# Kernel tuning notes

Measured on AMD Instinct MI355X. Metric: run time of the kernel, lower is better.

The kernel has to match this reference:

```python
import jax, jax.numpy as jnp
import numpy as np

S, B, D, H, F = 2048, 4, 1024, 16, 4096
DH = D // H  # per-head dim (nhid)
EPS = 1e-5


def layer_norm(x, g, b):
    m = jnp.mean(x, axis=-1, keepdims=True)
    v = jnp.mean((x - m) ** 2, axis=-1, keepdims=True)
    return (x - m) * jax.lax.rsqrt(v + EPS) * g + b


def setup_inputs() -> dict:
    key = jax.random.key(0)
    ks = jax.random.split(key, 16)
    s = 1.0 / np.sqrt(D)
    sf = 1.0 / np.sqrt(F)
    return {
        "x": jax.random.normal(ks[0], (S, B, D), dtype=jnp.float32),
        "ln1_g": jnp.ones((D,), jnp.float32),
        "ln1_b": jnp.zeros((D,), jnp.float32),
        "ln2_g": jnp.ones((D,), jnp.float32),
        "ln2_b": jnp.zeros((D,), jnp.float32),
        "Wq": jax.random.normal(ks[1], (D, D), jnp.float32) * s,
        "bq": jnp.zeros((D,), jnp.float32),
        "Wk": jax.random.normal(ks[2], (D, D), jnp.float32) * s,
        "bk": jnp.zeros((D,), jnp.float32),
        "Wv": jax.random.normal(ks[3], (D, D), jnp.float32) * s,
        "bv": jnp.zeros((D,), jnp.float32),
        "Wo": jax.random.normal(ks[4], (D, D), jnp.float32) * s,
        "bo": jnp.zeros((D,), jnp.float32),
        "W1": jax.random.normal(ks[5], (D, F), jnp.float32) * s,
        "b1": jnp.zeros((F,), jnp.float32),
        "W2": jax.random.normal(ks[6], (F, D), jnp.float32) * sf,
        "b2": jnp.zeros((D,), jnp.float32),
    }


def reference(x, ln1_g, ln1_b, ln2_g, ln2_b, Wq, bq, Wk, bk, Wv, bv, Wo, bo, W1, b1, W2, b2):
    # --- sublayer 0: LN -> full (non-causal) multi-head self-attention -> residual ---
    h = layer_norm(x, ln1_g, ln1_b)                      # [S,B,D]
    q = (h @ Wq + bq).reshape(S, B, H, DH)
    k = (h @ Wk + bk).reshape(S, B, H, DH)
    v = (h @ Wv + bv).reshape(S, B, H, DH)
    scale = 1.0 / jnp.sqrt(jnp.asarray(DH, x.dtype))
    scores = jnp.einsum("sbhd,tbhd->bhst", q, k) * scale  # [B,H,S,S]
    attn = jax.nn.softmax(scores, axis=-1)
    ctx = jnp.einsum("bhst,tbhd->sbhd", attn, v).reshape(S, B, D)
    x = x + (ctx @ Wo + bo)
    # --- sublayer 1: LN -> position-wise FFN -> residual ---
    h2 = layer_norm(x, ln2_g, ln2_b)
    ff = jax.nn.relu(h2 @ W1 + b1) @ W2 + b2
    return x + ff
```

## Files before the change

### kernel.cpp

```cpp
#include <hip/hip_runtime.h>
#include <hip/hip_bf16.h>
#include <stdint.h>

constexpr int S = 2048;
constexpr int B = 4;
constexpr int D = 1024;
constexpr int H = 16;
constexpr int F = 4096;
constexpr int DH = 64;
constexpr int N = S * B;
constexpr int QKVS = 3 * D;

typedef __attribute__((ext_vector_type(8))) short  bf16x8;
typedef __attribute__((ext_vector_type(4))) float  floatx4;

__device__ __forceinline__ unsigned short f2bf(float f) {
    __hip_bfloat16 h = __float2bfloat16(f);
    return __builtin_bit_cast(unsigned short, h);
}
__device__ __forceinline__ uint32_t pack_bf2_fast(float a, float b) {
    uint32_t ua = __builtin_bit_cast(uint32_t, a) + 0x8000u;
    uint32_t ub = __builtin_bit_cast(uint32_t, b) + 0x8000u;
    return (ua >> 16) | (ub & 0xffff0000u);
}
__device__ __forceinline__ void glds16(const unsigned short* g, unsigned short* l) {
    __builtin_amdgcn_global_load_lds((__attribute__((address_space(1))) void*)(g),
                                     (__attribute__((address_space(3))) void*)(l),
                                     16, 0, 0);
}

__global__ __launch_bounds__(256) void convert_transpose(
    const float* __restrict__ src, unsigned short* __restrict__ dst, int K, int M) {
    __shared__ float tile[32][33];
    const int m0 = blockIdx.x * 32;
    const int k0 = blockIdx.y * 32;
    const int tx = threadIdx.x;
    const int ty = threadIdx.y;
    #pragma unroll
    for (int i = 0; i < 32; i += 8)
        tile[ty + i][tx] = src[(size_t)(k0 + ty + i) * M + m0 + tx];
    __syncthreads();
    #pragma unroll
    for (int i = 0; i < 32; i += 8)
        dst[(size_t)(m0 + ty + i) * K + k0 + tx] = f2bf(tile[tx][ty + i]);
}

__global__ __launch_bounds__(256) void concat_bias(
    const float* __restrict__ bq, const float* __restrict__ bk,
    const float* __restrict__ bv, float* __restrict__ dst) {
    int i = blockIdx.x * 256 + threadIdx.x;
    float v = (i < 1024) ? bq[i] : (i < 2048 ? bk[i - 1024] : bv[i - 2048]);
    dst[i] = v;
}

__global__ __launch_bounds__(256) void transpose_v(
    const unsigned short* __restrict__ qkv, unsigned short* __restrict__ vt) {
    __shared__ unsigned short t[64][72];
    const int tid = threadIdx.x;
    const int s0 = blockIdx.x * 64;
    const int h  = blockIdx.y;
    const int b  = blockIdx.z;
    #pragma unroll
    for (int i = 0; i < 2; i++) {
        int c = i * 256 + tid;
        int row = c >> 3, off = (c & 7) * 8;
        *(uint4*)&t[row][off] =
            *(const uint4*)(qkv + ((size_t)(s0 + row) * B + b) * QKVS + 2048 + h * 64 + off);
    }
    __syncthreads();
    #pragma unroll
    for (int i = 0; i < 2; i++) {
        int c = i * 256 + tid;
        int dh = c >> 3, off = (c & 7) * 8;
        unsigned short tmp[8];
        #pragma unroll
        for (int j = 0; j < 8; j++) tmp[j] = t[off + j][dh];
        *(uint4*)(vt + ((size_t)((b * H + h) * 64 + dh)) * S + s0 + off) = *(uint4*)tmp;
    }
}

__global__ __launch_bounds__(256) void ln_kernel(
    const float* __restrict__ x, const float* __restrict__ g,
    const float* __restrict__ b, unsigned short* __restrict__ out) {
    const int row = blockIdx.x;
    const int tid = threadIdx.x;
    float4 v = ((const float4*)(x + (size_t)row * D))[tid];
    float s  = v.x + v.y + v.z + v.w;
    float ss = v.x * v.x + v.y * v.y + v.z * v.z + v.w * v.w;
    #pragma unroll
    for (int o = 32; o > 0; o >>= 1) {
        s  += __shfl_down(s,  o, 64);
        ss += __shfl_down(ss, o, 64);
    }
    __shared__ float red[8];
    __shared__ float mv[2];
    const int wv = tid >> 6, ln = tid & 63;
    if (ln == 0) { red[wv] = s; red[4 + wv] = ss; }
    __syncthreads();
    if (tid == 0) {
        float S2 = red[0] + red[1] + red[2] + red[3];
        float SS = red[4] + red[5] + red[6] + red[7];
        float mean = S2 * (1.0f / D);
        float var  = SS * (1.0f / D) - mean * mean;
        mv[0] = mean;
        mv[1] = rsqrtf(var + 1e-5f);
    }
    __syncthreads();
    const float mean = mv[0], inv = mv[1];
    float4 gv = ((const float4*)g)[tid];
    float4 bv = ((const float4*)b)[tid];
    ushort4 o4;
    o4.x = f2bf((v.x - mean) * inv * gv.x + bv.x);
    o4.y = f2bf((v.y - mean) * inv * gv.y + bv.y);
    o4.z = f2bf((v.z - mean) * inv * gv.z + bv.z);
    o4.w = f2bf((v.w - mean) * inv * gv.w + bv.w);
    ((ushort4*)(out + (size_t)row * D))[tid] = o4;
}

template <int RELU, int RESID, int OUT_BF16>
__global__ __launch_bounds__(256, 3) void gemm_bt(
    const unsigned short* __restrict__ A,
    const unsigned short* __restrict__ Bt,
    const float* __restrict__ bias,
    const float* __restrict__ resid,
    void* __restrict__ out,
    int M, int K) {
    __shared__ __align__(16) unsigned short As[128 * 64];
    __shared__ __align__(16) unsigned short Bs[128 * 64];

    const int tid  = threadIdx.x;
    const int lane = tid & 63;
    const int wave = tid >> 6;
    const int wr = (wave >> 1) * 64;
    const int wc = (wave & 1) * 64;
    const int n0 = blockIdx.y * 128;
    const int m0 = blockIdx.x * 128;
    const int quad = lane >> 4;
    const int r    = lane & 15;

    floatx4 acc[4][4] = {};

    const int l8  = lane >> 3;
    const int gch = ((lane & 7) ^ l8) * 8;
    const unsigned short* gA = A  + (size_t)(n0 + wave * 32 + l8) * K + gch;
    const unsigned short* gB = Bt + (size_t)(m0 + wave * 32 + l8) * K + gch;
    unsigned short* lA = As + wave * 32 * 64;
    unsigned short* lB = Bs + wave * 32 * 64;
    const size_t rowstep = (size_t)8 * K;

    for (int k0 = 0; k0 < K; k0 += 64) {
        __syncthreads();
        #pragma unroll
        for (int c = 0; c < 4; c++) glds16(gA + c * rowstep, lA + c * 512);
        #pragma unroll
        for (int c = 0; c < 4; c++) glds16(gB + c * rowstep, lB + c * 512);
        gA += 64; gB += 64;
        __syncthreads();

        #pragma unroll
        for (int kk = 0; kk < 2; kk++) {
            const int fc = ((kk * 4 + quad) ^ (r & 7)) * 8;
            bf16x8 af[4], bfr[4];
            #pragma unroll
            for (int i = 0; i < 4; i++)
                af[i] = *(const bf16x8*)&As[(wr + i * 16 + r) * 64 + fc];
            #pragma unroll
            for (int j = 0; j < 4; j++)
                bfr[j] = *(const bf16x8*)&Bs[(wc + j * 16 + r) * 64 + fc];
            #pragma unroll
            for (int i = 0; i < 4; i++)
                #pragma unroll
                for (int j = 0; j < 4; j++)
                    acc[i][j] = __builtin_amdgcn_mfma_f32_16x16x32_bf16(af[i], bfr[j], acc[i][j], 0, 0, 0);
        }
    }

    #pragma unroll
    for (int i = 0; i < 4; i++) {
        #pragma unroll
        for (int j = 0; j < 4; j++) {
            const int row = n0 + wr + i * 16 + quad * 4;
            const int col = m0 + wc + j * 16 + r;
            const float bcol = bias[col];
            #pragma unroll
            for (int rr = 0; rr < 4; rr++) {
                float val = acc[i][j][rr] + bcol;
                if constexpr (RESID) val += resid[(size_t)(row + rr) * M + col];
                if constexpr (RELU)  val = fmaxf(val, 0.0f);
                if constexpr (OUT_BF16)
                    ((unsigned short*)out)[(size_t)(row + rr) * M + col] = f2bf(val);
                else
                    ((float*)out)[(size_t)(row + rr) * M + col] = val;
            }
        }
    }
}

__global__ __launch_bounds__(256, 2) void flash_attn(
    const unsigned short* __restrict__ qkv,
    const unsigned short* __restrict__ vt,
    unsigned short* __restrict__ ctx) {
    constexpr int LQK = 72;
    constexpr int LP  = 136;
    constexpr float SCL = 0.18033688011112042f;

    __shared__ __align__(16) unsigned short Ks[128 * LQK];
    __shared__ __align__(16) unsigned short Ps[128 * LP];
    __shared__ __align__(16) unsigned short Vs[64 * 128];

    const int tid  = threadIdx.x;
    const int lane = tid & 63;
    const int wave = tid >> 6;
    const int quad = lane >> 4;
    const int r    = lane & 15;
    const int flat = blockIdx.x;
    const int xcd  = flat & 7;
    const int t0   = (flat >> 3) & 15;
    const int bh   = (flat >> 7) * 8 + xcd;
    const int b    = bh >> 4;
    const int h    = bh & 15;
    const int s0   = t0 * 128;
    const int wq0  = wave * 32;

    unsigned short* Qs = Ks;
    #pragma unroll
    for (int i = 0; i < 4; i++) {
        int c = i * 256 + tid;
        int row = c >> 3, off = (c & 7) * 8;
        *(uint4*)&Qs[row * LQK + off] =
            *(const uint4*)(qkv + ((size_t)(s0 + row) * B + b) * QKVS + h * 64 + off);
    }
    __syncthreads();
    bf16x8 qf[2][2];
    #pragma unroll
    for (int j = 0; j < 2; j++)
        #pragma unroll
        for (int kk = 0; kk < 2; kk++)
            qf[j][kk] = *(const bf16x8*)&Qs[(wq0 + j * 16 + r) * LQK + kk * 32 + quad * 8];

    const bf16x8 ones = {(short)0x3F80, (short)0x3F80, (short)0x3F80, (short)0x3F80,
                         (short)0x3F80, (short)0x3F80, (short)0x3F80, (short)0x3F80};

    uint4 kr[4];
    const unsigned short* kbase  = qkv + (size_t)b * QKVS + 1024 + h * 64;
    const unsigned short* vtbase = vt + (size_t)((b * H + h) * 64) * S;
    #pragma unroll
    for (int i = 0; i < 4; i++) {
        int c = i * 256 + tid;
        int row = c >> 3, off = (c & 7) * 8;
        kr[i] = *(const uint4*)(kbase + (size_t)row * B * QKVS + off);
    }

    const int vdh_lo = lane >> 4;

    floatx4 acc2[2][4] = {};
    floatx4 accD[2]    = {};

    for (int t = 0; t < S / 128; t++) {
        __syncthreads();
        {
            const unsigned short* vtt = vtbase + t * 128;
            #pragma unroll
            for (int c4 = 0; c4 < 4; c4++) {
                const int c   = wave * 4 + c4;
                const int dh  = 4 * c + vdh_lo;
                const int gch = (lane & 15) ^ (dh & 15);
                glds16(vtt + (size_t)dh * S + gch * 8, Vs + c * 512);
            }
        }
        #pragma unroll
        for (int i = 0; i < 4; i++) {
            int c = i * 256 + tid;
            int row = c >> 3, off = (c & 7) * 8;
            *(uint4*)&Ks[row * LQK + off] = kr[i];
        }
        __syncthreads();

        if (t + 1 < S / 128) {
            const size_t tb = (size_t)(t + 1) * 128;
            #pragma unroll
            for (int i = 0; i < 4; i++) {
                int c = i * 256 + tid;
                int row = c >> 3, off = (c & 7) * 8;
                kr[i] = *(const uint4*)(kbase + (tb + row) * B * QKVS + off);
            }
        }

        #pragma unroll
        for (int i = 0; i < 8; i++) {
            bf16x8 kf0 = *(const bf16x8*)&Ks[(i * 16 + r) * LQK + quad * 8];
            bf16x8 kf1 = *(const bf16x8*)&Ks[(i * 16 + r) * LQK + 32 + quad * 8];
            #pragma unroll
            for (int j = 0; j < 2; j++) {
                floatx4 sc = {};
                sc = __builtin_amdgcn_mfma_f32_16x16x32_bf16(kf0, qf[j][0], sc, 0, 0, 0);
                sc = __builtin_amdgcn_mfma_f32_16x16x32_bf16(kf1, qf[j][1], sc, 0, 0, 0);
                float p0 = exp2f(sc[0] * SCL);
                float p1 = exp2f(sc[1] * SCL);
                float p2 = exp2f(sc[2] * SCL);
                float p3 = exp2f(sc[3] * SCL);
                uint2 w;
                w.x = pack_bf2_fast(p0, p1);
                w.y = pack_bf2_fast(p2, p3);
                *(uint2*)&Ps[(wq0 + j * 16 + r) * LP + i * 16 + quad * 4] = w;
            }
        }

        #pragma unroll
        for (int s = 0; s < 4; s++) {
            bf16x8 a2[2];
            #pragma unroll
            for (int j = 0; j < 2; j++)
                a2[j] = *(const bf16x8*)&Ps[(wq0 + j * 16 + r) * LP + s * 32 + quad * 8];
            bf16x8 b2[4];
            #pragma unroll
            for (int jn = 0; jn < 4; jn++)
                b2[jn] = *(const bf16x8*)&Vs[(jn * 16 + r) * 128 + (((s * 4 + quad) ^ r) * 8)];
            #pragma unroll
            for (int j = 0; j < 2; j++) {
                #pragma unroll
                for (int jn = 0; jn < 4; jn++)
                    acc2[j][jn] = __builtin_amdgcn_mfma_f32_16x16x32_bf16(a2[j], b2[jn], acc2[j][jn], 0, 0, 0);
                accD[j] = __builtin_amdgcn_mfma_f32_16x16x32_bf16(a2[j], ones, accD[j], 0, 0, 0);
            }
        }
    }

    float inv[2][4];
    #pragma unroll
    for (int j = 0; j < 2; j++)
        #pragma unroll
        for (int rr = 0; rr < 4; rr++)
            inv[j][rr] = 1.0f / accD[j][rr];

    #pragma unroll
    for (int j = 0; j < 2; j++) {
        #pragma unroll
        for (int jn = 0; jn < 4; jn++) {
            #pragma unroll
            for (int rr = 0; rr < 4; rr++) {
                const int qrow = wq0 + j * 16 + quad * 4 + rr;
                const int dh   = jn * 16 + r;
                ctx[((size_t)(s0 + qrow) * B + b) * D + h * 64 + dh] =
                    f2bf(acc2[j][jn][rr] * inv[j][rr]);
            }
        }
    }
}

extern "C" void kernel_launch(void* const* d_in, const int* in_sizes, int n_in,
                              void* d_out, int out_size, void* d_ws, size_t ws_size,
                              hipStream_t stream) {
    const float* x    = (const float*)d_in[0];
    const float* ln1g = (const float*)d_in[1];
    const float* ln1b = (const float*)d_in[2];
    const float* ln2g = (const float*)d_in[3];
    const float* ln2b = (const float*)d_in[4];
    const float* Wq   = (const float*)d_in[5];
    const float* bq   = (const float*)d_in[6];
    const float* Wk   = (const float*)d_in[7];
    const float* bk   = (const float*)d_in[8];
    const float* Wv   = (const float*)d_in[9];
    const float* bv   = (const float*)d_in[10];
    const float* Wo   = (const float*)d_in[11];
    const float* bo   = (const float*)d_in[12];
    const float* W1   = (const float*)d_in[13];
    const float* b1   = (const float*)d_in[14];
    const float* W2   = (const float*)d_in[15];
    const float* b2   = (const float*)d_in[16];
    float* out = (float*)d_out;

    char* ws = (char*)d_ws;
    const size_t MB = 1ull << 20;
    unsigned short* wqkvT = (unsigned short*)(ws + 0 * MB);
    unsigned short* woT   = (unsigned short*)(ws + 6 * MB);
    unsigned short* w1T   = (unsigned short*)(ws + 8 * MB);
    unsigned short* w2T   = (unsigned short*)(ws + 16 * MB);
    unsigned short* h     = (unsigned short*)(ws + 24 * MB);
    unsigned short* qkv   = (unsigned short*)(ws + 40 * MB);
    unsigned short* ctx   = (unsigned short*)(ws + 88 * MB);
    float*          bqkv  = (float*)(ws + 88 * MB);
    float*          x1    = (float*)(ws + 104 * MB);
    unsigned short* vt    = (unsigned short*)(ws + 104 * MB);
    unsigned short* ff1   = qkv;
    unsigned short* h2    = h;

    const dim3 tb(32, 8);
    convert_transpose<<<dim3(D / 32, D / 32), tb, 0, stream>>>(Wq, wqkvT, D, D);
    convert_transpose<<<dim3(D / 32, D / 32), tb, 0, stream>>>(Wk, wqkvT + (size_t)D * D, D, D);
    convert_transpose<<<dim3(D / 32, D / 32), tb, 0, stream>>>(Wv, wqkvT + 2 * (size_t)D * D, D, D);
    convert_transpose<<<dim3(D / 32, D / 32), tb, 0, stream>>>(Wo, woT, D, D);
    convert_transpose<<<dim3(F / 32, D / 32), tb, 0, stream>>>(W1, w1T, D, F);
    convert_transpose<<<dim3(D / 32, F / 32), tb, 0, stream>>>(W2, w2T, F, D);
    concat_bias<<<12, 256, 0, stream>>>(bq, bk, bv, bqkv);

    ln_kernel<<<N, 256, 0, stream>>>(x, ln1g, ln1b, h);

    gemm_bt<0, 0, 1><<<dim3(3 * D / 128, N / 128), 256, 0, stream>>>(
        h, wqkvT, bqkv, nullptr, qkv, 3 * D, D);

    transpose_v<<<dim3(S / 64, H, B), 256, 0, stream>>>(qkv, vt);

    flash_attn<<<dim3((S / 128) * H * B), 256, 0, stream>>>(qkv, vt, ctx);

    const dim3 g1(D / 128, N / 128);
    gemm_bt<0, 1, 0><<<g1, 256, 0, stream>>>(ctx, woT, bo, x, x1, D, D);

    ln_kernel<<<N, 256, 0, stream>>>(x1, ln2g, ln2b, h2);

    gemm_bt<1, 0, 1><<<dim3(F / 128, N / 128), 256, 0, stream>>>(h2, w1T, b1, nullptr, ff1, F, D);

    gemm_bt<0, 1, 0><<<g1, 256, 0, stream>>>(ff1, w2T, b2, x1, out, D, F);
}
```

Measured before the change: 588.5 us.

## Double query tile per attention block, fold softmax scale into QKV GEMM, chunk P

The attention kernel now handles 256 query rows per block (64 per wave) instead of 128, which halves how often each K/V tile is loaded and doubles reuse of K and V fragments. The softmax scale (log2e/sqrt(dh)) moves into the QKV GEMM epilogue for Q columns, removing a multiply per score. P is now written and read in 32-key chunks interleaved with the PV MFMAs, so the P buffer shares shared memory with Q and V. In exchange each thread holds more accumulator registers, the grid has half as many blocks, and Q rounding to bf16 now happens after scaling.

```diff
diff --git a/kernel.cpp b/kernel.cpp
--- a/kernel.cpp
+++ b/kernel.cpp
@@ -28,6 +28,8 @@
                                      (__attribute__((address_space(3))) void*)(l),
                                      16, 0, 0);
 }
+
+constexpr float QSCL = 0.18033688011112042f;
 
 __global__ __launch_bounds__(256) void convert_transpose(
     const float* __restrict__ src, unsigned short* __restrict__ dst, int K, int M) {
@@ -117,7 +119,7 @@
     ((ushort4*)(out + (size_t)row * D))[tid] = o4;
 }
 
-template <int RELU, int RESID, int OUT_BF16>
+template <int RELU, int RESID, int OUT_BF16, int QSCALE = 0>
 __global__ __launch_bounds__(256, 3) void gemm_bt(
     const unsigned short* __restrict__ A,
     const unsigned short* __restrict__ Bt,
@@ -182,11 +184,13 @@
             const int row = n0 + wr + i * 16 + quad * 4;
             const int col = m0 + wc + j * 16 + r;
             const float bcol = bias[col];
+            const float cscale = (QSCALE && col < 1024) ? QSCL : 1.0f;
             #pragma unroll
             for (int rr = 0; rr < 4; rr++) {
                 float val = acc[i][j][rr] + bcol;
                 if constexpr (RESID) val += resid[(size_t)(row + rr) * M + col];
                 if constexpr (RELU)  val = fmaxf(val, 0.0f);
+                if constexpr (QSCALE) val *= cscale;
                 if constexpr (OUT_BF16)
                     ((unsigned short*)out)[(size_t)(row + rr) * M + col] = f2bf(val);
                 else
@@ -201,12 +205,13 @@
     const unsigned short* __restrict__ vt,
     unsigned short* __restrict__ ctx) {
     constexpr int LQK = 72;
-    constexpr int LP  = 136;
-    constexpr float SCL = 0.18033688011112042f;
+    constexpr int LQ  = 72;
+    constexpr int LP  = 40;
 
     __shared__ __align__(16) unsigned short Ks[128 * LQK];
-    __shared__ __align__(16) unsigned short Ps[128 * LP];
-    __shared__ __align__(16) unsigned short Vs[64 * 128];
+    __shared__ __align__(16) unsigned short smem2[18432];
+    unsigned short* Pc = smem2;
+    unsigned short* Vs = smem2 + 256 * LP;
 
     const int tid  = threadIdx.x;
     const int lane = tid & 63;
@@ -215,28 +220,27 @@
     const int r    = lane & 15;
     const int flat = blockIdx.x;
     const int xcd  = flat & 7;
-    const int t0   = (flat >> 3) & 15;
-    const int bh   = (flat >> 7) * 8 + xcd;
+    const int t0   = (flat >> 3) & 7;
+    const int bh   = (flat >> 6) * 8 + xcd;
     const int b    = bh >> 4;
     const int h    = bh & 15;
-    const int s0   = t0 * 128;
-    const int wq0  = wave * 32;
-
-    unsigned short* Qs = Ks;
-    #pragma unroll
-    for (int i = 0; i < 4; i++) {
+    const int s0   = t0 * 256;
+    const int wq0  = wave * 64;
+
+    #pragma unroll
+    for (int i = 0; i < 8; i++) {
         int c = i * 256 + tid;
         int row = c >> 3, off = (c & 7) * 8;
-        *(uint4*)&Qs[row * LQK + off] =
+        *(uint4*)&smem2[row * LQ + off] =
             *(const uint4*)(qkv + ((size_t)(s0 + row) * B + b) * QKVS + h * 64 + off);
     }
     __syncthreads();
-    bf16x8 qf[2][2];
-    #pragma unroll
-    for (int j = 0; j < 2; j++)
+    bf16x8 qf[4][2];
+    #pragma unroll
+    for (int j = 0; j < 4; j++)
         #pragma unroll
         for (int kk = 0; kk < 2; kk++)
-            qf[j][kk] = *(const bf16x8*)&Qs[(wq0 + j * 16 + r) * LQK + kk * 32 + quad * 8];
+            qf[j][kk] = *(const bf16x8*)&smem2[(wq0 + j * 16 + r) * LQ + kk * 32 + quad * 8];
 
     const bf16x8 ones = {(short)0x3F80, (short)0x3F80, (short)0x3F80, (short)0x3F80,
                          (short)0x3F80, (short)0x3F80, (short)0x3F80, (short)0x3F80};
@@ -253,8 +257,8 @@
 
     const int vdh_lo = lane >> 4;
 
-    floatx4 acc2[2][4] = {};
-    floatx4 accD[2]    = {};
+    floatx4 acc2[4][4] = {};
+    floatx4 accD[4]    = {};
 
     for (int t = 0; t < S / 128; t++) {
         __syncthreads();
@@ -287,37 +291,36 @@
         }
 
         #pragma unroll
-        for (int i = 0; i < 8; i++) {
-            bf16x8 kf0 = *(const bf16x8*)&Ks[(i * 16 + r) * LQK + quad * 8];
-            bf16x8 kf1 = *(const bf16x8*)&Ks[(i * 16 + r) * LQK + 32 + quad * 8];
-            #pragma unroll
-            for (int j = 0; j < 2; j++) {
-                floatx4 sc = {};
-                sc = __builtin_amdgcn_mfma_f32_16x16x32_bf16(kf0, qf[j][0], sc, 0, 0, 0);
-                sc = __builtin_amdgcn_mfma_f32_16x16x32_bf16(kf1, qf[j][1], sc, 0, 0, 0);
-                float p0 = exp2f(sc[0] * SCL);
-                float p1 = exp2f(sc[1] * SCL);
-                float p2 = exp2f(sc[2] * SCL);
-                float p3 = exp2f(sc[3] * SCL);
-                uint2 w;
-                w.x = pack_bf2_fast(p0, p1);
-                w.y = pack_bf2_fast(p2, p3);
-                *(uint2*)&Ps[(wq0 + j * 16 + r) * LP + i * 16 + quad * 4] = w;
-            }
-        }
-
-        #pragma unroll
         for (int s = 0; s < 4; s++) {
-            bf16x8 a2[2];
-            #pragma unroll
-            for (int j = 0; j < 2; j++)
-                a2[j] = *(const bf16x8*)&Ps[(wq0 + j * 16 + r) * LP + s * 32 + quad * 8];
-            bf16x8 b2[4];
+            #pragma unroll
+            for (int ii = 0; ii < 2; ii++) {
+                const int krow = (s * 32 + ii * 16 + r) * LQK;
+                bf16x8 kf0 = *(const bf16x8*)&Ks[krow + quad * 8];
+                bf16x8 kf1 = *(const bf16x8*)&Ks[krow + 32 + quad * 8];
+                #pragma unroll
+                for (int j = 0; j < 4; j++) {
+                    floatx4 sc = {};
+                    sc = __builtin_amdgcn_mfma_f32_16x16x32_bf16(kf0, qf[j][0], sc, 0, 0, 0);
+                    sc = __builtin_amdgcn_mfma_f32_16x16x32_bf16(kf1, qf[j][1], sc, 0, 0, 0);
+                    float p0 = exp2f(sc[0]);
+                    float p1 = exp2f(sc[1]);
+                    float p2 = exp2f(sc[2]);
+                    float p3 = exp2f(sc[3]);
+                    uint2 w;
+                    w.x = pack_bf2_fast(p0, p1);
+                    w.y = pack_bf2_fast(p2, p3);
+                    *(uint2*)&Pc[(wq0 + j * 16 + r) * LP + ii * 16 + quad * 4] = w;
+                }
+            }
+            bf16x8 a2[4], b2[4];
+            #pragma unroll
+            for (int j = 0; j < 4; j++)
+                a2[j] = *(const bf16x8*)&Pc[(wq0 + j * 16 + r) * LP + quad * 8];
             #pragma unroll
             for (int jn = 0; jn < 4; jn++)
                 b2[jn] = *(const bf16x8*)&Vs[(jn * 16 + r) * 128 + (((s * 4 + quad) ^ r) * 8)];
             #pragma unroll
-            for (int j = 0; j < 2; j++) {
+            for (int j = 0; j < 4; j++) {
                 #pragma unroll
                 for (int jn = 0; jn < 4; jn++)
                     acc2[j][jn] = __builtin_amdgcn_mfma_f32_16x16x32_bf16(a2[j], b2[jn], acc2[j][jn], 0, 0, 0);
@@ -326,15 +329,11 @@
         }
     }
 
-    float inv[2][4];
-    #pragma unroll
-    for (int j = 0; j < 2; j++)
-        #pragma unroll
-        for (int rr = 0; rr < 4; rr++)
-            inv[j][rr] = 1.0f / accD[j][rr];
-
-    #pragma unroll
-    for (int j = 0; j < 2; j++) {
+    #pragma unroll
+    for (int j = 0; j < 4; j++) {
+        float inv[4];
+        #pragma unroll
+        for (int rr = 0; rr < 4; rr++) inv[rr] = 1.0f / accD[j][rr];
         #pragma unroll
         for (int jn = 0; jn < 4; jn++) {
             #pragma unroll
@@ -342,7 +341,7 @@
                 const int qrow = wq0 + j * 16 + quad * 4 + rr;
                 const int dh   = jn * 16 + r;
                 ctx[((size_t)(s0 + qrow) * B + b) * D + h * 64 + dh] =
-                    f2bf(acc2[j][jn][rr] * inv[j][rr]);
+                    f2bf(acc2[j][jn][rr] * inv[rr]);
             }
         }
     }
@@ -396,12 +395,12 @@
 
     ln_kernel<<<N, 256, 0, stream>>>(x, ln1g, ln1b, h);
 
-    gemm_bt<0, 0, 1><<<dim3(3 * D / 128, N / 128), 256, 0, stream>>>(
+    gemm_bt<0, 0, 1, 1><<<dim3(3 * D / 128, N / 128), 256, 0, stream>>>(
         h, wqkvT, bqkv, nullptr, qkv, 3 * D, D);
 
     transpose_v<<<dim3(S / 64, H, B), 256, 0, stream>>>(qkv, vt);
 
-    flash_attn<<<dim3((S / 128) * H * B), 256, 0, stream>>>(qkv, vt, ctx);
+    flash_attn<<<dim3((S / 256) * H * B), 256, 0, stream>>>(qkv, vt, ctx);
 
     const dim3 g1(D / 128, N / 128);
     gemm_bt<0, 1, 0><<<g1, 256, 0, stream>>>(ctx, woT, bo, x, x1, D, D);
```

Result: faster. 546.5 us (-7.2%).
